# Performance work log

Measured on AMD Instinct MI355X. Metric: run time of the kernel, lower is better.

The kernel has to match this reference:

```python
import jax, jax.numpy as jnp
import numpy as np

# dims (Nemotron-H 8B class mamba mixer)
HID = 4096      # hidden_size
NH = 128        # mamba_num_heads
HD = 64         # mamba_head_dim
DIN = NH * HD   # intermediate_size = 8192
G = 8           # n_groups
N = 128         # ssm_state_size
K = 4           # conv_kernel
CS = 256        # chunk_size
EPS = 1e-5
GROUP_SIZE = DIN // G
CONV_DIM = DIN + 2 * G * N           # 10240
PROJ = DIN + CONV_DIM + NH           # 18560 = gate | xBC | dt


def segment_sum(x):
    """x: [..., k] -> [..., k, k]; out[i,j] = sum_{m=j+1..i} x[m], -inf above diag."""
    k = x.shape[-1]
    xe = jnp.broadcast_to(x[..., None], x.shape + (k,))
    xe = jnp.where(jnp.tril(jnp.ones((k, k), bool), -1), xe, 0.0)
    s = jnp.cumsum(xe, axis=-2)
    return jnp.where(jnp.tril(jnp.ones((k, k), bool), 0), s, -jnp.inf)


def setup_inputs() -> dict:
    key = jax.random.key(0)
    ks = jax.random.split(key, 9)
    std = 0.02
    return {
        "hidden_states": jax.random.normal(ks[0], (2, 2048, HID), jnp.float32),
        "in_proj_w": jax.random.normal(ks[1], (PROJ, HID), jnp.float32) * std,
        "conv_w": jax.random.normal(ks[2], (CONV_DIM, 1, K), jnp.float32) * 0.1,
        "conv_b": jax.random.normal(ks[3], (CONV_DIM,), jnp.float32) * 0.01,
        "dt_bias": jax.random.uniform(ks[4], (NH,), jnp.float32, -4.0, -2.0),
        "A_log": jnp.log(jax.random.uniform(ks[5], (NH,), jnp.float32, 1.0, 16.0)),
        "D": jnp.ones((NH,), jnp.float32),
        "norm_w": jnp.ones((DIN,), jnp.float32),
        "out_proj_w": jax.random.normal(ks[8], (HID, DIN), jnp.float32) * std,
    }


def reference(hidden_states, in_proj_w, conv_w, conv_b, dt_bias, A_log, D, norm_w, out_proj_w):
    b, l, _ = hidden_states.shape
    zxbcdt = hidden_states @ in_proj_w.T                       # [b,l,PROJ]
    gate = zxbcdt[..., :DIN]
    xBC = zxbcdt[..., DIN:DIN + CONV_DIM]
    dt = zxbcdt[..., DIN + CONV_DIM:]                          # [b,l,NH]

    # causal depthwise conv1d + silu
    conv = jax.lax.conv_general_dilated(
        jnp.transpose(xBC, (0, 2, 1)), conv_w, (1,), [(K - 1, 0)],
        feature_group_count=CONV_DIM, dimension_numbers=("NCH", "OIH", "NCH"))
    xBC = jax.nn.silu(jnp.transpose(conv + conv_b[None, :, None], (0, 2, 1)))

    x = xBC[..., :DIN].reshape(b, l, NH, HD)
    B = xBC[..., DIN:DIN + G * N].reshape(b, l, G, N)
    C = xBC[..., DIN + G * N:].reshape(b, l, G, N)
    B = jnp.repeat(B, NH // G, axis=2)                         # [b,l,NH,N]
    C = jnp.repeat(C, NH // G, axis=2)

    A = -jnp.exp(A_log)                                        # [NH]
    dt = jax.nn.softplus(dt + dt_bias)                         # [b,l,NH]; limit (0,inf) is a no-op

    pad = (CS - l % CS) % CS
    def padl(t):
        return jnp.pad(t, [(0, 0), (0, pad)] + [(0, 0)] * (t.ndim - 2))

    D_res = D[None, None, :, None] * padl(x)                   # [b,L,NH,HD]
    xs = x * dt[..., None]
    Adt = A[None, None, :] * dt                                # [b,l,NH]

    nc = (l + pad) // CS
    def chunk(t):
        return padl(t).reshape((b, nc, CS) + t.shape[2:])
    xs, B, C = chunk(xs), chunk(B), chunk(C)                   # [b,c,k,h,*]
    Ac = jnp.transpose(chunk(Adt), (0, 3, 1, 2))               # [b,h,c,k]
    A_cumsum = jnp.cumsum(Ac, axis=-1)

    # 1. intra-chunk (diagonal blocks)
    L = jnp.exp(segment_sum(Ac))                               # [b,h,c,k,k]
    Gm = jnp.einsum("bcihn,bcjhn->bhcij", C, B)
    Y_diag = jnp.einsum("bhcij,bcjhd->bcihd", Gm * L, xs)

    # 2. chunk states
    decay_states = jnp.exp(A_cumsum[..., -1:] - A_cumsum)      # [b,h,c,k]
    states = jnp.einsum("bckhn,bhck,bckhd->bchdn", B, decay_states, xs)

    # 3. inter-chunk recurrence
    A_tail = jnp.pad(A_cumsum[..., -1], ((0, 0), (0, 0), (1, 0)))
    decay_chunk = jnp.exp(segment_sum(A_tail))                 # [b,h,c+1,c+1]
    states = jnp.concatenate([jnp.zeros_like(states[:, :1]), states], axis=1)
    new_states = jnp.einsum("bhzc,bchdn->bzhdn", decay_chunk, states)
    states = new_states[:, :-1]                                # [b,c,h,d,n]

    # 4. state -> output
    state_decay = jnp.exp(A_cumsum)                            # [b,h,c,k]
    Y_off = jnp.einsum("bckhn,bchdn,bhck->bckhd", C, states, state_decay)

    y = (Y_diag + Y_off).reshape(b, l + pad, NH, HD) + D_res
    y = y[:, :l].reshape(b, l, DIN)

    # gated grouped RMSNorm
    y = y * jax.nn.silu(gate)
    yg = y.reshape(b, l, G, GROUP_SIZE)
    var = jnp.mean(yg * yg, axis=-1, keepdims=True)
    y = (yg * jax.lax.rsqrt(var + EPS)).reshape(b, l, DIN) * norm_w
    return y @ out_proj_w.T
```

## Files before the change

kernel.cpp:

```cpp
#include <hip/hip_runtime.h>
#include <hip/hip_bf16.h>
#include <math.h>

#define HID 4096
#define NH 128
#define HD 64
#define DIN 8192
#define G 8
#define NSTATE 128
#define CS 256
#define GROUP_SIZE 1024
#define CONV_DIM 10240
#define PROJ 18560
#define PROJ_PAD 18688
#define BATCH 2
#define SEQ 2048
#define NT (BATCH*SEQ)
#define NC 8
#define DTSK 16

typedef __attribute__((ext_vector_type(8))) short bf16x8;
typedef __attribute__((ext_vector_type(4))) float f32x4;
typedef __attribute__((ext_vector_type(8))) unsigned short u16x8;
typedef __attribute__((ext_vector_type(4))) unsigned short u16x4;

__device__ __forceinline__ float sigmoidf_(float x){ return 1.f/(1.f+expf(-x)); }
__device__ __forceinline__ float siluf_(float x){ return x*sigmoidf_(x); }
__device__ __forceinline__ float softplusf_(float x){ return (x>20.f)? x : log1pf(expf(x)); }
__device__ __forceinline__ float b2f(unsigned short u){ union{unsigned int i; float f;} x; x.i = ((unsigned int)u)<<16; return x.f; }
__device__ __forceinline__ unsigned short f2b(float f){ __hip_bfloat16 h = __float2bfloat16(f); return *(unsigned short*)&h; }

__device__ __forceinline__ void gload_lds16(const void* g, void* l) {
  __builtin_amdgcn_global_load_lds((const __attribute__((address_space(1))) unsigned int*)g,
                                   (__attribute__((address_space(3))) unsigned int*)l, 16, 0, 0);
}
__device__ __forceinline__ bf16x8 ld8bf(const __hip_bfloat16* p){ return *(const bf16x8*)p; }

__global__ __launch_bounds__(256)
void cast_f32_bf16_kernel(const float* __restrict__ in, __hip_bfloat16* __restrict__ out, size_t n8) {
  size_t i = (size_t)blockIdx.x * 256 + threadIdx.x;
  size_t stride = (size_t)gridDim.x * 256;
  for (; i < n8; i += stride) {
    const float4* p = (const float4*)(in + i*8);
    float4 a = p[0], b = p[1];
    union { __hip_bfloat16 h[8]; int4 v; } o;
    o.h[0]=__float2bfloat16(a.x); o.h[1]=__float2bfloat16(a.y);
    o.h[2]=__float2bfloat16(a.z); o.h[3]=__float2bfloat16(a.w);
    o.h[4]=__float2bfloat16(b.x); o.h[5]=__float2bfloat16(b.y);
    o.h[6]=__float2bfloat16(b.z); o.h[7]=__float2bfloat16(b.w);
    *(int4*)(out + i*8) = o.v;
  }
}

template<bool OUT_BF16, bool GUARD_N>
__global__ __launch_bounds__(512)
void gemm_bf16_256(const __hip_bfloat16* __restrict__ A, const __hip_bfloat16* __restrict__ B,
                   void* __restrict__ Cout, int M, int Nreal, int Npad, int K) {
  const int nMt = M >> 8, nNt = Npad >> 8;
  const int nwg = nMt * nNt;
  const int cpx = nwg >> 3;
  const int lin = blockIdx.x;
  const int swz = (lin & 7) * cpx + (lin >> 3);
  const int mt = swz % nMt, ntile = swz / nMt;
  const int rowBase = mt << 8;
  const int colBase = ntile << 8;

  __shared__ short As[4][8192];
  __shared__ short Bs[4][8192];

  const int tid = threadIdx.x;
  const int lane = tid & 63, wid = tid >> 6;
  const int wr = wid >> 2, wc = wid & 3;
  const int l15 = lane & 15, l4 = lane >> 4;

  const int r0 = tid >> 2,        c0 = (tid & 3) ^ ((r0 >> 1) & 3);
  const int r1 = (512+tid) >> 2,  c1 = ((512+tid) & 3) ^ ((r1 >> 1) & 3);
  const __hip_bfloat16* gA0 = A + (size_t)(rowBase + r0)*K + c0*8;
  const __hip_bfloat16* gA1 = A + (size_t)(rowBase + r1)*K + c1*8;
  const __hip_bfloat16* gB0 = B + (size_t)(colBase + r0)*K + c0*8;
  const __hip_bfloat16* gB1 = B + (size_t)(colBase + r1)*K + c1*8;
  const int ld0 = wid*512, ld1 = 4096 + wid*512;

#define STAGE_A(q, kt) do { \
    gload_lds16(gA0 + (size_t)(kt)*32, (void*)&As[q][ld0]); \
    gload_lds16(gA1 + (size_t)(kt)*32, (void*)&As[q][ld1]); \
  } while(0)
#define STAGE_B(q, kt) do { \
    gload_lds16(gB0 + (size_t)(kt)*32, (void*)&Bs[q][ld0]); \
    gload_lds16(gB1 + (size_t)(kt)*32, (void*)&Bs[q][ld1]); \
  } while(0)

  int aoff[8], boff[4];
  #pragma unroll
  for (int m=0;m<8;++m){ int r = wr*128 + m*16 + l15; aoff[m] = r*32 + ((l4 ^ ((r>>1)&3))*8); }
  #pragma unroll
  for (int n=0;n<4;++n){ int r = wc*64  + n*16 + l15; boff[n] = r*32 + ((l4 ^ ((r>>1)&3))*8); }

  f32x4 acc[8][4] = {};
  const int NKT = K >> 5;

  STAGE_A(0,0); STAGE_B(0,0);
  STAGE_A(1,1); STAGE_B(1,1);
  STAGE_A(2,2); STAGE_B(2,2);
  asm volatile("s_waitcnt vmcnt(8)" ::: "memory");
  __builtin_amdgcn_s_barrier();

  for (int t = 0; t < NKT; ++t) {
    const short* ab = &As[t&3][0];
    const short* bb = &Bs[t&3][0];
    const int q3 = (t+3)&3;
    bf16x8 a[4], b[4], a2[4];
    #pragma unroll
    for (int m=0;m<4;++m) a[m] = *(const bf16x8*)&ab[aoff[m]];
    #pragma unroll
    for (int n=0;n<4;++n) b[n] = *(const bf16x8*)&bb[boff[n]];
    if (t + 3 < NKT) STAGE_A(q3, t+3);
    __builtin_amdgcn_s_barrier();
    asm volatile("s_waitcnt lgkmcnt(0)" ::: "memory");
    __builtin_amdgcn_sched_barrier(0);
    __builtin_amdgcn_s_setprio(1);
    #pragma unroll
    for (int m=0;m<4;++m)
      #pragma unroll
      for (int n=0;n<4;++n)
        acc[m][n] = __builtin_amdgcn_mfma_f32_16x16x32_bf16(a[m], b[n], acc[m][n], 0, 0, 0);
    __builtin_amdgcn_s_setprio(0);
    __builtin_amdgcn_s_barrier();
    #pragma unroll
    for (int m=0;m<4;++m) a2[m] = *(const bf16x8*)&ab[aoff[m+4]];
    if (t + 3 < NKT) STAGE_B(q3, t+3);
    const int rem = NKT - 1 - t;
    if (rem >= 3)      asm volatile("s_waitcnt vmcnt(8)" ::: "memory");
    else if (rem == 2) asm volatile("s_waitcnt vmcnt(4)" ::: "memory");
    else if (rem == 1) asm volatile("s_waitcnt vmcnt(0)" ::: "memory");
    __builtin_amdgcn_s_barrier();
    asm volatile("s_waitcnt lgkmcnt(0)" ::: "memory");
    __builtin_amdgcn_sched_barrier(0);
    __builtin_amdgcn_s_setprio(1);
    #pragma unroll
    for (int m=0;m<4;++m)
      #pragma unroll
      for (int n=0;n<4;++n)
        acc[m+4][n] = __builtin_amdgcn_mfma_f32_16x16x32_bf16(a2[m], b[n], acc[m+4][n], 0, 0, 0);
    __builtin_amdgcn_s_setprio(0);
    __builtin_amdgcn_s_barrier();
  }
#undef STAGE_A
#undef STAGE_B

  #pragma unroll
  for (int m=0;m<8;++m) {
    int row0 = rowBase + wr*128 + m*16 + l4*4;
    #pragma unroll
    for (int n=0;n<4;++n) {
      int col = colBase + wc*64 + n*16 + l15;
      if (!GUARD_N || col < Nreal) {
        #pragma unroll
        for (int j=0;j<4;++j) {
          if (OUT_BF16)
            ((__hip_bfloat16*)Cout)[(size_t)(row0+j)*Nreal + col] = __float2bfloat16(acc[m][n][j]);
          else
            ((float*)Cout)[(size_t)(row0+j)*Nreal + col] = acc[m][n][j];
        }
      }
    }
  }
}

__global__ __launch_bounds__(256)
void dt_gemm_splitk(const float* __restrict__ A, const float* __restrict__ B,
                    float* __restrict__ partial) {
  __shared__ float As[16][132];
  __shared__ float Bs[16][132];
  const int tid = threadIdx.x;
  const int tx = tid & 15, ty = tid >> 4;
  const int rowBase = blockIdx.y * 128;
  const int k0 = blockIdx.x * (HID/DTSK);
  float acc[8][8] = {};
  for (int kt = k0; kt < k0 + HID/DTSK; kt += 16) {
    for (int e = tid; e < 128*16; e += 256) {
      int r = e >> 4, c = e & 15;
      As[c][r] = A[(size_t)(rowBase + r) * HID + kt + c];
      Bs[c][r] = B[(size_t)r * HID + kt + c];
    }
    __syncthreads();
    #pragma unroll
    for (int kk = 0; kk < 16; ++kk) {
      float a[8], bv[8];
      #pragma unroll
      for (int i = 0; i < 8; ++i) a[i] = As[kk][ty*8+i];
      #pragma unroll
      for (int j = 0; j < 8; ++j) bv[j] = Bs[kk][tx*8+j];
      #pragma unroll
      for (int i = 0; i < 8; ++i)
        #pragma unroll
        for (int j = 0; j < 8; ++j)
          acc[i][j] += a[i]*bv[j];
    }
    __syncthreads();
  }
  float* outp = partial + (size_t)blockIdx.x * NT * NH;
  for (int i = 0; i < 8; ++i) {
    size_t ro = (size_t)(rowBase + ty*8 + i) * NH + tx*8;
    #pragma unroll
    for (int j = 0; j < 8; ++j) outp[ro + j] = acc[i][j];
  }
}

__global__ __launch_bounds__(256)
void dt_reduce_kernel(const float* __restrict__ partial, float* __restrict__ dtb) {
  int idx = blockIdx.x*256 + threadIdx.x;
  float s = 0.f;
  #pragma unroll
  for (int sk = 0; sk < DTSK; ++sk) s += partial[(size_t)sk*NT*NH + idx];
  dtb[idx] = s;
}

__global__ __launch_bounds__(256)
void conv_silu_kernel(const __hip_bfloat16* __restrict__ zx, const float* __restrict__ w,
                      const float* __restrict__ bias,
                      __hip_bfloat16* __restrict__ xbf,
                      __hip_bfloat16* __restrict__ Bbf,
                      __hip_bfloat16* __restrict__ Cbf) {
  int idx = blockIdx.x * 256 + threadIdx.x;
  int c8 = idx % (CONV_DIM/8);
  int t  = idx / (CONV_DIM/8);
  int c0 = c8 * 8;
  int l = t & (SEQ-1);
  float acc[8];
  *(float4*)&acc[0] = *(const float4*)&bias[c0];
  *(float4*)&acc[4] = *(const float4*)&bias[c0+4];
  float4 wv[8];
  #pragma unroll
  for (int q=0;q<8;++q) wv[q] = *(const float4*)&w[(c0+q)*4];
  #pragma unroll
  for (int k=0;k<4;++k) {
    if (l - 3 + k >= 0) {
      u16x8 v = *(const u16x8*)&zx[(size_t)(t-3+k)*PROJ + DIN + c0];
      #pragma unroll
      for (int q=0;q<8;++q) acc[q] += b2f(v[q]) * ((const float*)&wv[q])[k];
    }
  }
  u16x8 o;
  #pragma unroll
  for (int q=0;q<8;++q) o[q] = f2b(siluf_(acc[q]));
  if (c0 < DIN) *(u16x8*)&xbf[(size_t)t*DIN + c0] = o;
  else if (c0 < DIN + G*NSTATE) *(u16x8*)&Bbf[(size_t)t*(G*NSTATE) + (c0 - DIN)] = o;
  else *(u16x8*)&Cbf[(size_t)t*(G*NSTATE) + (c0 - DIN - G*NSTATE)] = o;
}

__global__ __launch_bounds__(256)
void dt_scan_kernel(float* __restrict__ dtbuf, const float* __restrict__ dt_bias,
                    const float* __restrict__ A_log, float* __restrict__ Acs) {
  int bid = blockIdx.x;
  int c = bid % NC;
  int h = (bid / NC) % NH;
  int b = bid / (NC*NH);
  int k = threadIdx.x;
  int t = b*SEQ + c*CS + k;
  float raw = dtbuf[(size_t)t*NH + h] + dt_bias[h];
  float dtv = softplusf_(raw);
  dtbuf[(size_t)t*NH + h] = dtv;
  float adt = -expf(A_log[h]) * dtv;
  __shared__ float s[CS];
  s[k] = adt;
  __syncthreads();
  for (int off = 1; off < CS; off <<= 1) {
    float v = (k >= off) ? s[k-off] : 0.f;
    __syncthreads();
    s[k] += v;
    __syncthreads();
  }
  Acs[((size_t)(b*NH + h)*NC + c)*CS + k] = s[k];
}

__global__ __launch_bounds__(256)
void prep_xt_kernel(const __hip_bfloat16* __restrict__ xbf, const float* __restrict__ dt_sp,
                    const float* __restrict__ Acs,
                    __hip_bfloat16* __restrict__ xsT, __hip_bfloat16* __restrict__ xwT) {
  int tt = blockIdx.x;
  int h  = blockIdx.y;
  int t0 = tt*64;
  int b = t0 >> 11, cc = (t0 >> 8) & 7, k0 = t0 & 255;
  __shared__ unsigned short T[64][72];
  __shared__ float dts[64], ews[64];
  int tid = threadIdx.x;
  if (tid < 64) {
    int t = t0 + tid;
    dts[tid] = dt_sp[(size_t)t*NH + h];
    const float* acs = Acs + ((size_t)(b*NH+h)*NC + cc)*CS;
    ews[tid] = __expf(acs[CS-1] - acs[k0 + tid]);
  }
  #pragma unroll
  for (int it = 0; it < 2; ++it) {
    int r = tid >> 2;
    int c8 = (tid & 3) + it*4;
    u16x8 v = *(const u16x8*)&xbf[(size_t)(t0+r)*DIN + h*64 + c8*8];
    #pragma unroll
    for (int q=0;q<8;++q) T[c8*8+q][r] = v[q];
  }
  __syncthreads();
  #pragma unroll
  for (int it = 0; it < 2; ++it) {
    int ch = tid >> 2;
    int tc = (tid & 3) + it*4;
    u16x8 v = *(const u16x8*)&T[ch][tc*8];
    u16x8 a, wv;
    #pragma unroll
    for (int q=0;q<8;++q) {
      float f = b2f(v[q]);
      float fs = f * dts[tc*8+q];
      a[q]  = f2b(fs);
      wv[q] = f2b(fs * ews[tc*8+q]);
    }
    *(u16x8*)&xsT[(size_t)(h*64+ch)*NT + t0 + tc*8] = a;
    *(u16x8*)&xwT[(size_t)(h*64+ch)*NT + t0 + tc*8] = wv;
  }
}

__global__ __launch_bounds__(256)
void transpose_bf16_kernel(const __hip_bfloat16* __restrict__ src, __hip_bfloat16* __restrict__ dst, int S) {
  int tt = blockIdx.x;
  int ct = blockIdx.y;
  int t0 = tt*64, c0 = ct*64;
  __shared__ unsigned short T[64][72];
  int tid = threadIdx.x;
  #pragma unroll
  for (int it = 0; it < 2; ++it) {
    int r = tid >> 2;
    int c8 = (tid & 3) + it*4;
    u16x8 v = *(const u16x8*)&src[(size_t)(t0+r)*S + c0 + c8*8];
    #pragma unroll
    for (int q=0;q<8;++q) T[c8*8+q][r] = v[q];
  }
  __syncthreads();
  #pragma unroll
  for (int it = 0; it < 2; ++it) {
    int ch = tid >> 2;
    int tc = (tid & 3) + it*4;
    u16x8 v = *(const u16x8*)&T[ch][tc*8];
    *(u16x8*)&dst[(size_t)(c0+ch)*NT + t0 + tc*8] = v;
  }
}

__global__ __launch_bounds__(256)
void chunk_states_mfma(const __hip_bfloat16* __restrict__ xwT, const __hip_bfloat16* __restrict__ BT,
                       float* __restrict__ states) {
  int h = blockIdx.x, bc = blockIdx.y;
  int g = h >> 4;
  int b = bc >> 3, c = bc & 7;
  int tbase = b*SEQ + c*CS;
  int tid = threadIdx.x, lane = tid & 63, w = tid >> 6;
  int l15 = lane & 15, l4 = lane >> 4;
  int n0 = w*32;
  const __hip_bfloat16* xp = xwT + (size_t)(h*64 + l15)*NT + tbase + l4*8;
  const __hip_bfloat16* bp = BT + (size_t)(g*128 + n0 + l15)*NT + tbase + l4*8;
  f32x4 acc[4][2] = {};
  for (int kc = 0; kc < 8; ++kc) {
    bf16x8 xf[4], bf2[2];
    #pragma unroll
    for (int tm=0;tm<4;++tm) xf[tm] = ld8bf(xp + (size_t)(tm*16)*NT + kc*32);
    #pragma unroll
    for (int tn=0;tn<2;++tn) bf2[tn] = ld8bf(bp + (size_t)(tn*16)*NT + kc*32);
    #pragma unroll
    for (int tm=0;tm<4;++tm)
      #pragma unroll
      for (int tn=0;tn<2;++tn)
        acc[tm][tn] = __builtin_amdgcn_mfma_f32_16x16x32_bf16(xf[tm], bf2[tn], acc[tm][tn], 0, 0, 0);
  }
  float* out = states + ((size_t)bc*NH + h)*(HD*NSTATE);
  #pragma unroll
  for (int tm=0;tm<4;++tm)
    #pragma unroll
    for (int tn=0;tn<2;++tn)
      #pragma unroll
      for (int q=0;q<4;++q)
        out[(size_t)(tm*16 + l4*4 + q)*NSTATE + n0 + tn*16 + l15] = acc[tm][tn][q];
}

__global__ void state_recurrence_kernel(const float* __restrict__ states, const float* __restrict__ Acs,
                                        __hip_bfloat16* __restrict__ states_bf) {
  int idx = blockIdx.x*256 + threadIdx.x;
  int dn = idx & 8191;
  int h = (idx >> 13) & 127;
  int b = idx >> 20;
  float S = 0.f;
  for (int c = 0; c < NC; ++c) {
    size_t off = ((size_t)(b*NC + c)*NH + h)*8192 + dn;
    float v = states[off];
    states_bf[off] = __float2bfloat16(S);
    float decay = expf(Acs[((size_t)(b*NH+h)*NC + c)*CS + CS-1]);
    S = S*decay + v;
  }
}

__global__ __launch_bounds__(256)
void y_mfma_kernel(const __hip_bfloat16* __restrict__ zx,
                   const __hip_bfloat16* __restrict__ Cn,
                   const __hip_bfloat16* __restrict__ Bn,
                   const __hip_bfloat16* __restrict__ xsT,
                   const __hip_bfloat16* __restrict__ Sbf,
                   const float* __restrict__ dt_sp,
                   const float* __restrict__ Acs,
                   const float* __restrict__ Dp,
                   __hip_bfloat16* __restrict__ ybf) {
  int h = blockIdx.x;
  int bc = blockIdx.y;
  int c = bc & 7, b = bc >> 3;
  int g = h >> 4;
  int tbase = b*SEQ + c*CS;
  int tid = threadIdx.x, lane = tid & 63, w = tid >> 6;
  int l15 = lane & 15, l4 = lane >> 4;
  int i0 = w*64;
  __shared__ float acs_s[CS];
  __shared__ unsigned short P[4][64][72];
  acs_s[tid] = Acs[((size_t)(b*NH+h)*NC + c)*CS + tid];
  __syncthreads();

  float acs_i[4], rd[4];
  float Dh = Dp[h];
  #pragma unroll
  for (int ti=0;ti<4;++ti) {
    int ig = i0 + ti*16 + l15;
    acs_i[ti] = acs_s[ig];
    rd[ti] = Dh / dt_sp[(size_t)(tbase+ig)*NH + h];
  }
  const __hip_bfloat16* Cbase = Cn + (size_t)tbase*1024 + g*128;
  const __hip_bfloat16* Bbase = Bn + (size_t)tbase*1024 + g*128;
  const __hip_bfloat16* xbase = xsT + (size_t)(h*64 + l15)*NT + tbase;

  f32x4 accY[4][4] = {};
  for (int jb = 0; jb < 4; ++jb) {
    int j0 = jb*64;
    f32x4 sacc[4][4] = {};
    for (int kc = 0; kc < 4; ++kc) {
      bf16x8 bfr[4], cfr[4];
      #pragma unroll
      for (int tj=0;tj<4;++tj) bfr[tj] = ld8bf(Bbase + (size_t)(j0 + tj*16 + l15)*1024 + kc*32 + l4*8);
      #pragma unroll
      for (int ti=0;ti<4;++ti) cfr[ti] = ld8bf(Cbase + (size_t)(i0 + ti*16 + l15)*1024 + kc*32 + l4*8);
      #pragma unroll
      for (int tj=0;tj<4;++tj)
        #pragma unroll
        for (int ti=0;ti<4;++ti)
          sacc[tj][ti] = __builtin_amdgcn_mfma_f32_16x16x32_bf16(bfr[tj], cfr[ti], sacc[tj][ti], 0, 0, 0);
    }
    #pragma unroll
    for (int tj=0;tj<4;++tj)
      #pragma unroll
      for (int ti=0;ti<4;++ti) {
        int ig = i0 + ti*16 + l15;
        float ai = acs_i[ti];
        u16x4 pk;
        #pragma unroll
        for (int q=0;q<4;++q) {
          int jg = j0 + tj*16 + l4*4 + q;
          float v = (jg <= ig) ? sacc[tj][ti][q] * __expf(ai - acs_s[jg]) : 0.f;
          if (jg == ig) v += rd[ti];
          pk[q] = f2b(v);
        }
        *(u16x4*)&P[w][ti*16 + l15][tj*16 + l4*4] = pk;
      }
    #pragma unroll
    for (int kc2 = 0; kc2 < 2; ++kc2) {
      bf16x8 xf[4], pf[4];
      #pragma unroll
      for (int tm=0;tm<4;++tm) xf[tm] = ld8bf(xbase + (size_t)(tm*16)*NT + j0 + kc2*32 + l4*8);
      #pragma unroll
      for (int ti=0;ti<4;++ti) pf[ti] = *(const bf16x8*)&P[w][ti*16 + l15][kc2*32 + l4*8];
      #pragma unroll
      for (int tm=0;tm<4;++tm)
        #pragma unroll
        for (int ti=0;ti<4;++ti)
          accY[tm][ti] = __builtin_amdgcn_mfma_f32_16x16x32_bf16(xf[tm], pf[ti], accY[tm][ti], 0, 0, 0);
    }
  }
  const __hip_bfloat16* Sb = Sbf + ((size_t)bc*NH + h)*(HD*NSTATE);
  f32x4 oacc[4][4] = {};
  for (int kc = 0; kc < 4; ++kc) {
    bf16x8 sf[4], cfr[4];
    #pragma unroll
    for (int tm=0;tm<4;++tm) sf[tm] = ld8bf(Sb + (size_t)(tm*16 + l15)*NSTATE + kc*32 + l4*8);
    #pragma unroll
    for (int ti=0;ti<4;++ti) cfr[ti] = ld8bf(Cbase + (size_t)(i0 + ti*16 + l15)*1024 + kc*32 + l4*8);
    #pragma unroll
    for (int tm=0;tm<4;++tm)
      #pragma unroll
      for (int ti=0;ti<4;++ti)
        oacc[tm][ti] = __builtin_amdgcn_mfma_f32_16x16x32_bf16(sf[tm], cfr[ti], oacc[tm][ti], 0, 0, 0);
  }
  #pragma unroll
  for (int ti=0;ti<4;++ti) {
    int ig = i0 + ti*16 + l15;
    int t = tbase + ig;
    float sd = __expf(acs_i[ti]);
    #pragma unroll
    for (int tm=0;tm<4;++tm) {
      int ch0 = h*64 + tm*16 + l4*4;
      u16x4 gv = *(const u16x4*)&zx[(size_t)t*PROJ + ch0];
      u16x4 out;
      #pragma unroll
      for (int q=0;q<4;++q) {
        float yv = accY[tm][ti][q] + sd * oacc[tm][ti][q];
        yv *= siluf_(b2f(gv[q]));
        out[q] = f2b(yv);
      }
      *(u16x4*)&ybf[(size_t)t*DIN + ch0] = out;
    }
  }
}

__global__ __launch_bounds__(256)
void groupnorm_bf16_kernel(unsigned short* __restrict__ y, const float* __restrict__ norm_w) {
  int bid = blockIdx.x;
  int g = bid % G;
  int t = bid / G;
  unsigned short* yp = y + (size_t)t*DIN + g*GROUP_SIZE;
  int tid = threadIdx.x;
  u16x4 v = *(const u16x4*)&yp[tid*4];
  float f[4]; float ss = 0.f;
  #pragma unroll
  for (int j=0;j<4;++j) { f[j] = b2f(v[j]); ss += f[j]*f[j]; }
  #pragma unroll
  for (int off = 32; off > 0; off >>= 1) ss += __shfl_xor(ss, off);
  __shared__ float wsum[4];
  int wave = tid >> 6;
  if ((tid & 63) == 0) wsum[wave] = ss;
  __syncthreads();
  float tot = wsum[0]+wsum[1]+wsum[2]+wsum[3];
  float rs = rsqrtf(tot/(float)GROUP_SIZE + 1e-5f);
  const float* nw = norm_w + g*GROUP_SIZE + tid*4;
  u16x4 o;
  #pragma unroll
  for (int j=0;j<4;++j) o[j] = f2b(f[j] * rs * nw[j]);
  *(u16x4*)&yp[tid*4] = o;
}

extern "C" void kernel_launch(void* const* d_in, const int* in_sizes, int n_in,
                              void* d_out, int out_size, void* d_ws, size_t ws_size,
                              hipStream_t stream) {
  const float* hs        = (const float*)d_in[0];
  const float* in_proj_w = (const float*)d_in[1];
  const float* conv_w    = (const float*)d_in[2];
  const float* conv_b    = (const float*)d_in[3];
  const float* dt_bias   = (const float*)d_in[4];
  const float* A_log     = (const float*)d_in[5];
  const float* Dp        = (const float*)d_in[6];
  const float* norm_w    = (const float*)d_in[7];
  const float* out_proj_w= (const float*)d_in[8];
  float* outp = (float*)d_out;

  char* ws = (char*)d_ws;
  __hip_bfloat16* zx_bf = (__hip_bfloat16*)ws;
  char* p = ws + (size_t)NT*PROJ*2;
  __hip_bfloat16* x_bf  = (__hip_bfloat16*)p; p += (size_t)NT*DIN*2;
  __hip_bfloat16* B_bf  = (__hip_bfloat16*)p; p += (size_t)NT*G*NSTATE*2;
  __hip_bfloat16* C_bf  = (__hip_bfloat16*)p; p += (size_t)NT*G*NSTATE*2;
  __hip_bfloat16* BT    = (__hip_bfloat16*)p; p += (size_t)NT*G*NSTATE*2;
  float* states = (float*)p;  p += (size_t)BATCH*NC*NH*HD*NSTATE*4;
  __hip_bfloat16* y_bf  = (__hip_bfloat16*)p; p += (size_t)NT*DIN*2;
  float* dtb    = (float*)p;  p += (size_t)NT*NH*4;
  float* Acs    = (float*)p;  p += (size_t)BATCH*NH*NC*CS*4;
  float* dt_part = (float*)y_bf;
  char* F = p;
  __hip_bfloat16* w_in_bf   = (__hip_bfloat16*)F;
  __hip_bfloat16* xsT       = (__hip_bfloat16*)F;
  __hip_bfloat16* xwT       = (__hip_bfloat16*)(F + 67108864);
  __hip_bfloat16* hs_bf     = (__hip_bfloat16*)(F + 153092096);
  __hip_bfloat16* states_bf = (__hip_bfloat16*)(F + 153092096);
  char* F2 = F + 153092096 + 33554432;
  __hip_bfloat16* w_out_bf  = (__hip_bfloat16*)F2;

  dt_gemm_splitk<<<dim3(DTSK, NT/128), 256, 0, stream>>>(hs, in_proj_w + (size_t)(DIN+CONV_DIM)*HID, dt_part);
  dt_reduce_kernel<<<(NT*NH)/256, 256, 0, stream>>>(dt_part, dtb);

  cast_f32_bf16_kernel<<<2048, 256, 0, stream>>>(hs, hs_bf, (size_t)NT*HID/8);
  cast_f32_bf16_kernel<<<2048, 256, 0, stream>>>(in_proj_w, w_in_bf, (size_t)PROJ*HID/8);
  hipMemsetAsync(w_in_bf + (size_t)PROJ*HID, 0, (size_t)(PROJ_PAD - PROJ)*HID*2, stream);
  cast_f32_bf16_kernel<<<2048, 256, 0, stream>>>(out_proj_w, w_out_bf, (size_t)HID*DIN/8);

  gemm_bf16_256<true, true><<<dim3((NT/256)*(PROJ_PAD/256)), 512, 0, stream>>>(
      hs_bf, w_in_bf, zx_bf, NT, PROJ, PROJ_PAD, HID);

  conv_silu_kernel<<<(NT*CONV_DIM/8)/256, 256, 0, stream>>>(zx_bf, conv_w, conv_b, x_bf, B_bf, C_bf);
  dt_scan_kernel<<<BATCH*NH*NC, CS, 0, stream>>>(dtb, dt_bias, A_log, Acs);
  prep_xt_kernel<<<dim3(NT/64, NH), 256, 0, stream>>>(x_bf, dtb, Acs, xsT, xwT);
  transpose_bf16_kernel<<<dim3(NT/64, (G*NSTATE)/64), 256, 0, stream>>>(B_bf, BT, G*NSTATE);
  chunk_states_mfma<<<dim3(NH, BATCH*NC), 256, 0, stream>>>(xwT, BT, states);
  state_recurrence_kernel<<<(BATCH*NH*HD*NSTATE)/256, 256, 0, stream>>>(states, Acs, states_bf);
  y_mfma_kernel<<<dim3(NH, BATCH*NC), 256, 0, stream>>>(zx_bf, C_bf, B_bf, xsT, states_bf, dtb, Acs, Dp, y_bf);
  groupnorm_bf16_kernel<<<NT*G, 256, 0, stream>>>((unsigned short*)y_bf, norm_w);

  gemm_bf16_256<false, false><<<dim3((NT/256)*(HID/256)), 512, 0, stream>>>(
      y_bf, w_out_bf, outp, NT, HID, HID, DIN);
}
```

Before: 1.866 ms.

## Restructure GEMM main loop into unrolled ping-pong with prefetched LDS fragments

Rewrites the bf16 GEMM k-loop into a two-step unrolled schedule where LDS fragment reads for the next MFMA half are issued before the current MFMA batch. This halves barriers per tile and overlaps LDS reads with compute. Prefetch depth drops from three stages to two, and launch_bounds now requests two blocks per CU, which constrains registers. Risks are spills from the doubled fragment registers and less latency hiding for global loads.

```diff
diff --git a/kernel.cpp b/kernel.cpp
--- a/kernel.cpp
+++ b/kernel.cpp
@@ -53,7 +53,7 @@
 }
 
 template<bool OUT_BF16, bool GUARD_N>
-__global__ __launch_bounds__(512)
+__global__ __launch_bounds__(512, 2)
 void gemm_bf16_256(const __hip_bfloat16* __restrict__ A, const __hip_bfloat16* __restrict__ B,
                    void* __restrict__ Cout, int M, int Nreal, int Npad, int K) {
   const int nMt = M >> 8, nNt = Npad >> 8;
@@ -81,14 +81,16 @@
   const __hip_bfloat16* gB1 = B + (size_t)(colBase + r1)*K + c1*8;
   const int ld0 = wid*512, ld1 = 4096 + wid*512;
 
-#define STAGE_A(q, kt) do { \
+#define STAGE(q, kt) do { \
     gload_lds16(gA0 + (size_t)(kt)*32, (void*)&As[q][ld0]); \
     gload_lds16(gA1 + (size_t)(kt)*32, (void*)&As[q][ld1]); \
-  } while(0)
-#define STAGE_B(q, kt) do { \
     gload_lds16(gB0 + (size_t)(kt)*32, (void*)&Bs[q][ld0]); \
     gload_lds16(gB1 + (size_t)(kt)*32, (void*)&Bs[q][ld1]); \
   } while(0)
+#define LGKM0_FENCE() do { \
+    asm volatile("s_waitcnt lgkmcnt(0)" ::: "memory"); \
+    __builtin_amdgcn_sched_barrier(0); \
+  } while(0)
 
   int aoff[8], boff[4];
   #pragma unroll
@@ -99,54 +101,89 @@
   f32x4 acc[8][4] = {};
   const int NKT = K >> 5;
 
-  STAGE_A(0,0); STAGE_B(0,0);
-  STAGE_A(1,1); STAGE_B(1,1);
-  STAGE_A(2,2); STAGE_B(2,2);
-  asm volatile("s_waitcnt vmcnt(8)" ::: "memory");
+  STAGE(0, 0);
+  STAGE(1, 1);
+  asm volatile("s_waitcnt vmcnt(4)" ::: "memory");
   __builtin_amdgcn_s_barrier();
-
-  for (int t = 0; t < NKT; ++t) {
-    const short* ab = &As[t&3][0];
-    const short* bb = &Bs[t&3][0];
-    const int q3 = (t+3)&3;
-    bf16x8 a[4], b[4], a2[4];
-    #pragma unroll
-    for (int m=0;m<4;++m) a[m] = *(const bf16x8*)&ab[aoff[m]];
-    #pragma unroll
-    for (int n=0;n<4;++n) b[n] = *(const bf16x8*)&bb[boff[n]];
-    if (t + 3 < NKT) STAGE_A(q3, t+3);
+  bf16x8 aP[4], bP[4], aQ[4], bQ[4];
+  {
+    const short* ab = &As[0][0]; const short* bb = &Bs[0][0];
+    #pragma unroll
+    for (int m=0;m<4;++m) aP[m] = *(const bf16x8*)&ab[aoff[m]];
+    #pragma unroll
+    for (int n=0;n<4;++n) bP[n] = *(const bf16x8*)&bb[boff[n]];
+  }
+
+  for (int u = 0; u < NKT/2; ++u) {
+    const int t0 = 2*u, t1 = 2*u + 1;
+    if (t0 + 2 < NKT) STAGE((t0+2)&3, t0+2);
+    LGKM0_FENCE();
+    bf16x8 a2[4];
+    { const short* ab = &As[t0&3][0];
+      #pragma unroll
+      for (int m=0;m<4;++m) a2[m] = *(const bf16x8*)&ab[aoff[m+4]];
+    }
+    __builtin_amdgcn_s_setprio(1);
+    #pragma unroll
+    for (int m=0;m<4;++m)
+      #pragma unroll
+      for (int n=0;n<4;++n)
+        acc[m][n] = __builtin_amdgcn_mfma_f32_16x16x32_bf16(aP[m], bP[n], acc[m][n], 0, 0, 0);
+    __builtin_amdgcn_s_setprio(0);
+    if (t0 + 2 < NKT) asm volatile("s_waitcnt vmcnt(4)" ::: "memory");
+    else              asm volatile("s_waitcnt vmcnt(0)" ::: "memory");
     __builtin_amdgcn_s_barrier();
-    asm volatile("s_waitcnt lgkmcnt(0)" ::: "memory");
-    __builtin_amdgcn_sched_barrier(0);
+    LGKM0_FENCE();
+    { const short* ab = &As[t1&3][0]; const short* bb = &Bs[t1&3][0];
+      #pragma unroll
+      for (int m=0;m<4;++m) aQ[m] = *(const bf16x8*)&ab[aoff[m]];
+      #pragma unroll
+      for (int n=0;n<4;++n) bQ[n] = *(const bf16x8*)&bb[boff[n]];
+    }
     __builtin_amdgcn_s_setprio(1);
     #pragma unroll
     for (int m=0;m<4;++m)
       #pragma unroll
       for (int n=0;n<4;++n)
-        acc[m][n] = __builtin_amdgcn_mfma_f32_16x16x32_bf16(a[m], b[n], acc[m][n], 0, 0, 0);
+        acc[m+4][n] = __builtin_amdgcn_mfma_f32_16x16x32_bf16(a2[m], bP[n], acc[m+4][n], 0, 0, 0);
     __builtin_amdgcn_s_setprio(0);
-    __builtin_amdgcn_s_barrier();
-    #pragma unroll
-    for (int m=0;m<4;++m) a2[m] = *(const bf16x8*)&ab[aoff[m+4]];
-    if (t + 3 < NKT) STAGE_B(q3, t+3);
-    const int rem = NKT - 1 - t;
-    if (rem >= 3)      asm volatile("s_waitcnt vmcnt(8)" ::: "memory");
-    else if (rem == 2) asm volatile("s_waitcnt vmcnt(4)" ::: "memory");
-    else if (rem == 1) asm volatile("s_waitcnt vmcnt(0)" ::: "memory");
-    __builtin_amdgcn_s_barrier();
-    asm volatile("s_waitcnt lgkmcnt(0)" ::: "memory");
-    __builtin_amdgcn_sched_barrier(0);
+    if (t1 + 2 < NKT) STAGE((t1+2)&3, t1+2);
+    LGKM0_FENCE();
+    bf16x8 a2b[4];
+    { const short* ab = &As[t1&3][0];
+      #pragma unroll
+      for (int m=0;m<4;++m) a2b[m] = *(const bf16x8*)&ab[aoff[m+4]];
+    }
     __builtin_amdgcn_s_setprio(1);
     #pragma unroll
     for (int m=0;m<4;++m)
       #pragma unroll
       for (int n=0;n<4;++n)
-        acc[m+4][n] = __builtin_amdgcn_mfma_f32_16x16x32_bf16(a2[m], b[n], acc[m+4][n], 0, 0, 0);
+        acc[m][n] = __builtin_amdgcn_mfma_f32_16x16x32_bf16(aQ[m], bQ[n], acc[m][n], 0, 0, 0);
     __builtin_amdgcn_s_setprio(0);
-    __builtin_amdgcn_s_barrier();
-  }
-#undef STAGE_A
-#undef STAGE_B
+    if (t1 + 1 < NKT) {
+      if (t1 + 2 < NKT) asm volatile("s_waitcnt vmcnt(4)" ::: "memory");
+      else              asm volatile("s_waitcnt vmcnt(0)" ::: "memory");
+      __builtin_amdgcn_s_barrier();
+      LGKM0_FENCE();
+      const short* ab = &As[(t1+1)&3][0]; const short* bb = &Bs[(t1+1)&3][0];
+      #pragma unroll
+      for (int m=0;m<4;++m) aP[m] = *(const bf16x8*)&ab[aoff[m]];
+      #pragma unroll
+      for (int n=0;n<4;++n) bP[n] = *(const bf16x8*)&bb[boff[n]];
+    } else {
+      LGKM0_FENCE();
+    }
+    __builtin_amdgcn_s_setprio(1);
+    #pragma unroll
+    for (int m=0;m<4;++m)
+      #pragma unroll
+      for (int n=0;n<4;++n)
+        acc[m+4][n] = __builtin_amdgcn_mfma_f32_16x16x32_bf16(a2b[m], bQ[n], acc[m+4][n], 0, 0, 0);
+    __builtin_amdgcn_s_setprio(0);
+  }
+#undef STAGE
+#undef LGKM0_FENCE
 
   #pragma unroll
   for (int m=0;m<8;++m) {
```

Measured after the change: 1.991 ms. 6.7% more time.
